# Kernel tuning notes

Measured on AMD Instinct MI355X. Metric: run time of the kernel, lower is better.

## Reference

```python
import jax, jax.numpy as jnp
import numpy as np

NUM_HEADS = 16
HEAD_DIM = 64  # hidden 1024 / 16 heads


def setup_inputs() -> dict:
    key = jax.random.key(0)
    ks = jax.random.split(key, 4)
    B, S, D = 2, 2048, 1024
    scale = 1.0 / np.sqrt(D)
    return {
        "hidden_states": jax.random.normal(ks[0], (B, S, D), jnp.float32),
        "Wq": jax.random.normal(ks[1], (D, D), jnp.float32) * scale,
        "bq": jnp.zeros((D,), jnp.float32),
        "Wk": jax.random.normal(ks[2], (D, D), jnp.float32) * scale,
        "bk": jnp.zeros((D,), jnp.float32),
        "Wv": jax.random.normal(ks[3], (D, D), jnp.float32) * scale,
        "bv": jnp.zeros((D,), jnp.float32),
    }


def _split_heads(x):
    B, S, D = x.shape
    return x.reshape(B, S, NUM_HEADS, HEAD_DIM).transpose(0, 2, 1, 3)  # [B,H,S,dh]


def reference(hidden_states, Wq, bq, Wk, bk, Wv, bv):
    q = _split_heads(hidden_states @ Wq + bq)
    k = _split_heads(hidden_states @ Wk + bk)
    v = _split_heads(hidden_states @ Wv + bv)
    scores = jnp.einsum("bhqd,bhkd->bhqk", q, k) / jnp.sqrt(
        jnp.asarray(HEAD_DIM, hidden_states.dtype))
    probs = jax.nn.softmax(scores, axis=-1)  # dropout is identity in eval mode
    ctx = jnp.einsum("bhqk,bhkd->bhqd", probs, v)
    B, H, S, dh = ctx.shape
    return ctx.transpose(0, 2, 1, 3).reshape(B, S, H * dh)
```

## Files before the change

### kernel.cpp

```cpp
#include <hip/hip_runtime.h>
#include <hip/hip_bf16.h>


typedef __attribute__((ext_vector_type(8))) short bf16x8;
typedef __attribute__((ext_vector_type(4))) float f32x4;
typedef __attribute__((ext_vector_type(4))) int int4v;

#define MFMA16(A, B, C) __builtin_amdgcn_mfma_f32_16x16x32_bf16((A), (B), (C), 0, 0, 0)

#if __has_builtin(__builtin_amdgcn_exp2f)
#define EXP2(x) __builtin_amdgcn_exp2f(x)
#else
#define EXP2(x) exp2f(x)
#endif

static __device__ __forceinline__ unsigned short f2bf(float f) {
    union { float f; unsigned int u; } v;
    v.f = f;
    unsigned int u = v.u;
    u += ((u >> 16) & 1u) + 0x7FFFu;
    return (unsigned short)(u >> 16);
}

static __device__ __forceinline__ void gload_lds16(const void* g, void* l) {
    __builtin_amdgcn_global_load_lds(
        (const __attribute__((address_space(1))) void*)g,
        (__attribute__((address_space(3))) void*)l, 16, 0, 0);
}

__global__ __launch_bounds__(256) void cast_hs(const float* __restrict__ in,
                                               unsigned short* __restrict__ out) {
    const size_t i = ((size_t)blockIdx.x * 256 + threadIdx.x) * 8;
    float4 a0 = *reinterpret_cast<const float4*>(in + i);
    float4 a1 = *reinterpret_cast<const float4*>(in + i + 4);
    unsigned short t[8];
    t[0] = f2bf(a0.x); t[1] = f2bf(a0.y); t[2] = f2bf(a0.z); t[3] = f2bf(a0.w);
    t[4] = f2bf(a1.x); t[5] = f2bf(a1.y); t[6] = f2bf(a1.z); t[7] = f2bf(a1.w);
    *reinterpret_cast<int4v*>(out + i) = *reinterpret_cast<int4v*>(t);
}

__global__ __launch_bounds__(256) void transpose_cast_w(
    const float* __restrict__ W0, const float* __restrict__ W1,
    const float* __restrict__ W2, unsigned short* __restrict__ Wt) {
    __shared__ float Ts[64][65];
    const float* W = (blockIdx.z == 0) ? W0 : (blockIdx.z == 1) ? W1 : W2;
    unsigned short* O = Wt + (size_t)blockIdx.z * 1048576;

    const int t  = threadIdx.x;
    const int k0 = blockIdx.y * 64;
    const int n0 = blockIdx.x * 64;

    {
        const int kr = t >> 2, nc = (t & 3) * 16;
        const float* p = W + (size_t)(k0 + kr) * 1024 + n0 + nc;
        float4 r0 = *reinterpret_cast<const float4*>(p);
        float4 r1 = *reinterpret_cast<const float4*>(p + 4);
        float4 r2 = *reinterpret_cast<const float4*>(p + 8);
        float4 r3 = *reinterpret_cast<const float4*>(p + 12);
        float* d = &Ts[kr][nc];
        d[0]=r0.x; d[1]=r0.y; d[2]=r0.z; d[3]=r0.w;
        d[4]=r1.x; d[5]=r1.y; d[6]=r1.z; d[7]=r1.w;
        d[8]=r2.x; d[9]=r2.y; d[10]=r2.z; d[11]=r2.w;
        d[12]=r3.x; d[13]=r3.y; d[14]=r3.z; d[15]=r3.w;
    }
    __syncthreads();
    {
        const int nr = t >> 2, kc = (t & 3) * 16;
        unsigned short tmp[16];
#pragma unroll
        for (int i = 0; i < 16; i++) tmp[i] = f2bf(Ts[kc + i][nr]);
        unsigned short* d = O + (size_t)(n0 + nr) * 1024 + k0 + kc;
        *reinterpret_cast<int4v*>(d)     = *reinterpret_cast<int4v*>(&tmp[0]);
        *reinterpret_cast<int4v*>(d + 8) = *reinterpret_cast<int4v*>(&tmp[8]);
    }
}

__global__ __launch_bounds__(256) void qkv_gemm_dma(
    const unsigned short* __restrict__ hsb,
    const unsigned short* __restrict__ Wt,
    const float* __restrict__ b0, const float* __restrict__ b1,
    const float* __restrict__ b2,
    unsigned short* __restrict__ Qo,
    unsigned short* __restrict__ Ko,
    unsigned short* __restrict__ Vto)
{
    __shared__ unsigned short As[128][32];
    __shared__ unsigned short Bs[128][32];

    const int z = blockIdx.z;
    const unsigned short* W = Wt + (size_t)z * 1048576;
    const float* bias = (z == 0) ? b0 : (z == 1) ? b1 : b2;

    const int tid  = threadIdx.x;
    const int lane = tid & 63;
    const int w    = tid >> 6;
    const int l15  = lane & 15;
    const int quad = lane >> 4;
    const int m0   = blockIdx.y * 128;
    const int n0   = blockIdx.x * 128;
    const int wm   = (w >> 1) * 64;
    const int wn   = (w & 1) * 64;

    const int drow = lane >> 2;
    const int dcol = (lane & 3) * 8;

    f32x4 acc[4][4];
#pragma unroll
    for (int i = 0; i < 4; i++)
#pragma unroll
        for (int j = 0; j < 4; j++)
            acc[i][j] = (f32x4){0.f, 0.f, 0.f, 0.f};

    for (int k0 = 0; k0 < 1024; k0 += 32) {
        __syncthreads();
#pragma unroll
        for (int p = 0; p < 2; p++) {
            const int s = w * 2 + p;
            gload_lds16(hsb + (size_t)(m0 + s * 16 + drow) * 1024 + k0 + dcol,
                        &As[s * 16][0]);
            gload_lds16(W   + (size_t)(n0 + s * 16 + drow) * 1024 + k0 + dcol,
                        &Bs[s * 16][0]);
        }
        __syncthreads();

        bf16x8 af[4], bfr[4];
#pragma unroll
        for (int i = 0; i < 4; i++)
            af[i] = *reinterpret_cast<const bf16x8*>(&As[wm + i * 16 + l15][quad * 8]);
#pragma unroll
        for (int j = 0; j < 4; j++)
            bfr[j] = *reinterpret_cast<const bf16x8*>(&Bs[wn + j * 16 + l15][quad * 8]);
#pragma unroll
        for (int i = 0; i < 4; i++)
#pragma unroll
            for (int j = 0; j < 4; j++)
                acc[i][j] = MFMA16(af[i], bfr[j], acc[i][j]);
    }

    if (z == 0) {
        const float qs = 0.18033688f;
#pragma unroll
        for (int i = 0; i < 4; i++) {
            const int mbase = m0 + wm + i * 16 + quad * 4;
#pragma unroll
            for (int j = 0; j < 4; j++) {
                const int n = n0 + wn + j * 16 + l15;
                const int h = n >> 6, d = n & 63;
                const float bn = bias[n];
#pragma unroll
                for (int r = 0; r < 4; r++) {
                    const int mm = mbase + r;
                    const int b = mm >> 11, s = mm & 2047;
                    Qo[(((size_t)(b * 16 + h) * 2048 + s) * 64) + d] =
                        f2bf((acc[i][j][r] + bn) * qs);
                }
            }
        }
    } else if (z == 1) {
#pragma unroll
        for (int i = 0; i < 4; i++) {
            const int mbase = m0 + wm + i * 16 + quad * 4;
#pragma unroll
            for (int j = 0; j < 4; j++) {
                const int n = n0 + wn + j * 16 + l15;
                const int h = n >> 6, d = n & 63;
                const float bn = bias[n];
#pragma unroll
                for (int r = 0; r < 4; r++) {
                    const int mm = mbase + r;
                    const int b = mm >> 11, s = mm & 2047;
                    const int dsw = ((((d >> 3) ^ (s & 7)) & 7) << 3) | (d & 7);
                    Ko[(((size_t)(b * 16 + h) * 2048 + s) * 64) + dsw] =
                        f2bf(acc[i][j][r] + bn);
                }
            }
        }
    } else {
#pragma unroll
        for (int i = 0; i < 4; i++) {
            const int mbase = m0 + wm + i * 16 + quad * 4;
            const int b = mbase >> 11, s0 = mbase & 2047;
#pragma unroll
            for (int j = 0; j < 4; j++) {
                const int n = n0 + wn + j * 16 + l15;
                const int h = n >> 6, d = n & 63;
                const float bn = bias[n];
                ushort4 v4;
                v4.x = f2bf(acc[i][j][0] + bn);
                v4.y = f2bf(acc[i][j][1] + bn);
                v4.z = f2bf(acc[i][j][2] + bn);
                v4.w = f2bf(acc[i][j][3] + bn);
                const int cs  = (s0 & 63) >> 3;
                const int ssw = (s0 & ~63) | (((cs ^ (d & 7)) & 7) << 3) | (s0 & 7);
                *reinterpret_cast<ushort4*>(
                    Vto + ((size_t)(b * 16 + h) * 64 + d) * 2048 + ssw) = v4;
            }
        }
    }
}

__global__ __launch_bounds__(256) void attn3(
    const unsigned short* __restrict__ Qg,
    const unsigned short* __restrict__ Kg,
    const unsigned short* __restrict__ Vtg,
    float* __restrict__ out)
{
    __shared__ unsigned short Ks[64][64];
    __shared__ unsigned short Vs[64][64];
    __shared__ unsigned short Ps[4][16][66];

    const int tid  = threadIdx.x;
    const int lane = tid & 63;
    const int w    = tid >> 6;
    const int l15  = lane & 15;
    const int quad = lane >> 4;

    const int q0 = blockIdx.x * 64;
    const int h  = blockIdx.y;
    const int b  = blockIdx.z;
    const size_t base = (size_t)(b * 16 + h) * 2048 * 64;
    const unsigned short* Qh  = Qg  + base;
    const unsigned short* Kh  = Kg  + base;
    const unsigned short* Vth = Vtg + base;

    const int drow = lane >> 3;
    const int dcol = (lane & 7) * 8;

    bf16x8 qf[2];
#pragma unroll
    for (int ks = 0; ks < 2; ks++)
        qf[ks] = *reinterpret_cast<const bf16x8*>(
            Qh + (size_t)(q0 + w * 16 + l15) * 64 + ks * 32 + quad * 8);

    f32x4 o[4];
#pragma unroll
    for (int t = 0; t < 4; t++) o[t] = (f32x4){0.f, 0.f, 0.f, 0.f};
    float rsum[4] = {0.f, 0.f, 0.f, 0.f};

    const int c0 = (((quad + 0) ^ (l15 & 7)) & 7) * 8;
    const int c1 = (((quad + 4) ^ (l15 & 7)) & 7) * 8;

    for (int kt = 0; kt < 32; kt++) {
        __syncthreads();
#pragma unroll
        for (int p = 0; p < 2; p++) {
            const int s = w * 2 + p;
            gload_lds16(Kh  + (size_t)kt * 4096 + (size_t)(s * 8 + drow) * 64 + dcol,
                        &Ks[s * 8][0]);
            gload_lds16(Vth + (size_t)(s * 8 + drow) * 2048 + kt * 64 + dcol,
                        &Vs[s * 8][0]);
        }
        __syncthreads();

#pragma unroll
        for (int t = 0; t < 4; t++) {
            f32x4 sc = (f32x4){0.f, 0.f, 0.f, 0.f};
            {
                bf16x8 kf = *reinterpret_cast<const bf16x8*>(&Ks[t * 16 + l15][c0]);
                sc = MFMA16(qf[0], kf, sc);
            }
            {
                bf16x8 kf = *reinterpret_cast<const bf16x8*>(&Ks[t * 16 + l15][c1]);
                sc = MFMA16(qf[1], kf, sc);
            }
#pragma unroll
            for (int r = 0; r < 4; r++) {
                const float p = EXP2(sc[r]);
                rsum[r] += p;
                Ps[w][quad * 4 + r][t * 16 + l15] = f2bf(p);
            }
        }

        __builtin_amdgcn_wave_barrier();

        bf16x8 pf[2];
#pragma unroll
        for (int ks = 0; ks < 2; ks++)
            pf[ks] = *reinterpret_cast<const bf16x8*>(&Ps[w][l15][ks * 32 + quad * 8]);
#pragma unroll
        for (int t = 0; t < 4; t++) {
            {
                bf16x8 vf = *reinterpret_cast<const bf16x8*>(&Vs[t * 16 + l15][c0]);
                o[t] = MFMA16(pf[0], vf, o[t]);
            }
            {
                bf16x8 vf = *reinterpret_cast<const bf16x8*>(&Vs[t * 16 + l15][c1]);
                o[t] = MFMA16(pf[1], vf, o[t]);
            }
        }
    }

#pragma unroll
    for (int off = 1; off < 16; off <<= 1)
#pragma unroll
        for (int r = 0; r < 4; r++)
            rsum[r] += __shfl_xor(rsum[r], off, 64);

#pragma unroll
    for (int t = 0; t < 4; t++) {
#pragma unroll
        for (int r = 0; r < 4; r++) {
            const int q = q0 + w * 16 + quad * 4 + r;
            const size_t oidx = (((size_t)b * 2048 + q) * 16 + h) * 64 + t * 16 + l15;
            out[oidx] = o[t][r] / rsum[r];
        }
    }
}

__global__ void fill_sentinel(float* out, int n, float pat) {
    int i = blockIdx.x * blockDim.x + threadIdx.x;
    if (i < n) out[i] = pat;
}

extern "C" void kernel_launch(void* const* d_in, const int* in_sizes, int n_in,
                              void* d_out, int out_size, void* d_ws, size_t ws_size,
                              hipStream_t stream) {
    const size_t n_hs  = (size_t)4096 * 1024;
    const size_t n_w   = (size_t)1024 * 1024;
    const size_t n_qkv = n_hs;
    const size_t need = (n_hs + 3 * n_w + 3 * n_qkv) * sizeof(unsigned short);

    bool order_ok = (n_in == 7) &&
        in_sizes[0] == 4194304 &&
        in_sizes[1] == 1048576 && in_sizes[2] == 1024 &&
        in_sizes[3] == 1048576 && in_sizes[4] == 1024 &&
        in_sizes[5] == 1048576 && in_sizes[6] == 1024;
    if (!order_ok || out_size != 4194304) {
        fill_sentinel<<<(out_size + 255) / 256, 256, 0, stream>>>(
            (float*)d_out, out_size, 4.0f);
        return;
    }
    if (ws_size < need) {
        fill_sentinel<<<(out_size + 255) / 256, 256, 0, stream>>>(
            (float*)d_out, out_size, 2.0f);
        return;
    }

    const float* hs = (const float*)d_in[0];
    const float* Wq = (const float*)d_in[1];
    const float* bq = (const float*)d_in[2];
    const float* Wk = (const float*)d_in[3];
    const float* bk = (const float*)d_in[4];
    const float* Wv = (const float*)d_in[5];
    const float* bv = (const float*)d_in[6];

    unsigned short* hsb = (unsigned short*)d_ws;
    unsigned short* Wt  = hsb + n_hs;
    unsigned short* Q   = Wt + 3 * n_w;
    unsigned short* K   = Q + n_qkv;
    unsigned short* Vt  = K + n_qkv;

    cast_hs<<<2048, 256, 0, stream>>>(hs, hsb);
    transpose_cast_w<<<dim3(16, 16, 3), 256, 0, stream>>>(Wq, Wk, Wv, Wt);

    dim3 g1(8, 32, 3);
    qkv_gemm_dma<<<g1, dim3(256), 0, stream>>>(hsb, Wt, bq, bk, bv, Q, K, Vt);

    dim3 g2(32, 16, 2);
    attn3<<<g2, dim3(256), 0, stream>>>(Q, K, Vt, (float*)d_out);
}
```

Baseline: 202.2 us.

## Widen GEMM and attention K tiles, pre-swizzle operands to avoid LDS conflicts

The QKV GEMM K-step grows from 32 to 64. The bf16 hidden states and transposed weights are now written with an XOR column swizzle, so the GEMM's LDS fragment reads avoid bank conflicts. The attention kernel loads 128 keys per tile instead of 64, which halves the number of block barriers. The bf16 rounding also drops round-to-nearest-even for a simpler round-half-up, which slightly changes numerics. Larger LDS tiles may lower occupancy.

Measured after the change: 204.8 us. No clear change (+1.3%).

```diff
diff --git a/kernel.cpp b/kernel.cpp
--- a/kernel.cpp
+++ b/kernel.cpp
@@ -17,9 +17,7 @@
 static __device__ __forceinline__ unsigned short f2bf(float f) {
     union { float f; unsigned int u; } v;
     v.f = f;
-    unsigned int u = v.u;
-    u += ((u >> 16) & 1u) + 0x7FFFu;
-    return (unsigned short)(u >> 16);
+    return (unsigned short)((v.u + 0x8000u) >> 16);
 }
 
 static __device__ __forceinline__ void gload_lds16(const void* g, void* l) {
@@ -30,13 +28,17 @@
 
 __global__ __launch_bounds__(256) void cast_hs(const float* __restrict__ in,
                                                unsigned short* __restrict__ out) {
-    const size_t i = ((size_t)blockIdx.x * 256 + threadIdx.x) * 8;
-    float4 a0 = *reinterpret_cast<const float4*>(in + i);
-    float4 a1 = *reinterpret_cast<const float4*>(in + i + 4);
+    const size_t flat = ((size_t)blockIdx.x * 256 + threadIdx.x) * 8;
+    const int m = (int)(flat >> 10);
+    const int k = (int)(flat & 1023);
+    float4 a0 = *reinterpret_cast<const float4*>(in + flat);
+    float4 a1 = *reinterpret_cast<const float4*>(in + flat + 4);
     unsigned short t[8];
     t[0] = f2bf(a0.x); t[1] = f2bf(a0.y); t[2] = f2bf(a0.z); t[3] = f2bf(a0.w);
     t[4] = f2bf(a1.x); t[5] = f2bf(a1.y); t[6] = f2bf(a1.z); t[7] = f2bf(a1.w);
-    *reinterpret_cast<int4v*>(out + i) = *reinterpret_cast<int4v*>(t);
+    const int csw = (((k >> 3) & 7) ^ (m & 7)) << 3;
+    *reinterpret_cast<int4v*>(out + (size_t)m * 1024 + (k & ~63) + csw) =
+        *reinterpret_cast<int4v*>(t);
 }
 
 __global__ __launch_bounds__(256) void transpose_cast_w(
@@ -69,9 +71,11 @@
         unsigned short tmp[16];
 #pragma unroll
         for (int i = 0; i < 16; i++) tmp[i] = f2bf(Ts[kc + i][nr]);
-        unsigned short* d = O + (size_t)(n0 + nr) * 1024 + k0 + kc;
-        *reinterpret_cast<int4v*>(d)     = *reinterpret_cast<int4v*>(&tmp[0]);
-        *reinterpret_cast<int4v*>(d + 8) = *reinterpret_cast<int4v*>(&tmp[8]);
+        unsigned short* base = O + (size_t)(n0 + nr) * 1024 + k0;
+        const int c0 = ((kc >> 3) ^ (nr & 7)) & 7;
+        const int c1 = (((kc >> 3) + 1) ^ (nr & 7)) & 7;
+        *reinterpret_cast<int4v*>(base + c0 * 8) = *reinterpret_cast<int4v*>(&tmp[0]);
+        *reinterpret_cast<int4v*>(base + c1 * 8) = *reinterpret_cast<int4v*>(&tmp[8]);
     }
 }
 
@@ -84,8 +88,8 @@
     unsigned short* __restrict__ Ko,
     unsigned short* __restrict__ Vto)
 {
-    __shared__ unsigned short As[128][32];
-    __shared__ unsigned short Bs[128][32];
+    __shared__ unsigned short As[128][64];
+    __shared__ unsigned short Bs[128][64];
 
     const int z = blockIdx.z;
     const unsigned short* W = Wt + (size_t)z * 1048576;
@@ -101,8 +105,8 @@
     const int wm   = (w >> 1) * 64;
     const int wn   = (w & 1) * 64;
 
-    const int drow = lane >> 2;
-    const int dcol = (lane & 3) * 8;
+    const int drow = lane >> 3;
+    const int dcol = (lane & 7) * 8;
 
     f32x4 acc[4][4];
 #pragma unroll
@@ -111,30 +115,36 @@
         for (int j = 0; j < 4; j++)
             acc[i][j] = (f32x4){0.f, 0.f, 0.f, 0.f};
 
-    for (int k0 = 0; k0 < 1024; k0 += 32) {
+    const int l7 = l15 & 7;
+
+    for (int k0 = 0; k0 < 1024; k0 += 64) {
         __syncthreads();
 #pragma unroll
-        for (int p = 0; p < 2; p++) {
-            const int s = w * 2 + p;
-            gload_lds16(hsb + (size_t)(m0 + s * 16 + drow) * 1024 + k0 + dcol,
-                        &As[s * 16][0]);
-            gload_lds16(W   + (size_t)(n0 + s * 16 + drow) * 1024 + k0 + dcol,
-                        &Bs[s * 16][0]);
+        for (int p = 0; p < 4; p++) {
+            const int seg = w * 4 + p;
+            gload_lds16(hsb + (size_t)(m0 + seg * 8 + drow) * 1024 + k0 + dcol,
+                        &As[seg * 8][0]);
+            gload_lds16(W   + (size_t)(n0 + seg * 8 + drow) * 1024 + k0 + dcol,
+                        &Bs[seg * 8][0]);
         }
         __syncthreads();
 
-        bf16x8 af[4], bfr[4];
-#pragma unroll
-        for (int i = 0; i < 4; i++)
-            af[i] = *reinterpret_cast<const bf16x8*>(&As[wm + i * 16 + l15][quad * 8]);
-#pragma unroll
-        for (int j = 0; j < 4; j++)
-            bfr[j] = *reinterpret_cast<const bf16x8*>(&Bs[wn + j * 16 + l15][quad * 8]);
-#pragma unroll
-        for (int i = 0; i < 4; i++)
+#pragma unroll
+        for (int kk = 0; kk < 64; kk += 32) {
+            const int csw = ((((kk >> 3) + quad) ^ l7) & 7) * 8;
+            bf16x8 af[4], bfr[4];
+#pragma unroll
+            for (int i = 0; i < 4; i++)
+                af[i] = *reinterpret_cast<const bf16x8*>(&As[wm + i * 16 + l15][csw]);
 #pragma unroll
             for (int j = 0; j < 4; j++)
-                acc[i][j] = MFMA16(af[i], bfr[j], acc[i][j]);
+                bfr[j] = *reinterpret_cast<const bf16x8*>(&Bs[wn + j * 16 + l15][csw]);
+#pragma unroll
+            for (int i = 0; i < 4; i++)
+#pragma unroll
+                for (int j = 0; j < 4; j++)
+                    acc[i][j] = MFMA16(af[i], bfr[j], acc[i][j]);
+        }
     }
 
     if (z == 0) {
@@ -199,14 +209,14 @@
     }
 }
 
-__global__ __launch_bounds__(256) void attn3(
+__global__ __launch_bounds__(256) void attn4(
     const unsigned short* __restrict__ Qg,
     const unsigned short* __restrict__ Kg,
     const unsigned short* __restrict__ Vtg,
     float* __restrict__ out)
 {
-    __shared__ unsigned short Ks[64][64];
-    __shared__ unsigned short Vs[64][64];
+    __shared__ unsigned short Ks[128][64];
+    __shared__ unsigned short Vs[64][128];
     __shared__ unsigned short Ps[4][16][66];
 
     const int tid  = threadIdx.x;
@@ -223,9 +233,6 @@
     const unsigned short* Kh  = Kg  + base;
     const unsigned short* Vth = Vtg + base;
 
-    const int drow = lane >> 3;
-    const int dcol = (lane & 7) * 8;
-
     bf16x8 qf[2];
 #pragma unroll
     for (int ks = 0; ks < 2; ks++)
@@ -240,53 +247,64 @@
     const int c0 = (((quad + 0) ^ (l15 & 7)) & 7) * 8;
     const int c1 = (((quad + 4) ^ (l15 & 7)) & 7) * 8;
 
-    for (int kt = 0; kt < 32; kt++) {
+    for (int kt = 0; kt < 16; kt++) {
         __syncthreads();
 #pragma unroll
-        for (int p = 0; p < 2; p++) {
-            const int s = w * 2 + p;
-            gload_lds16(Kh  + (size_t)kt * 4096 + (size_t)(s * 8 + drow) * 64 + dcol,
-                        &Ks[s * 8][0]);
-            gload_lds16(Vth + (size_t)(s * 8 + drow) * 2048 + kt * 64 + dcol,
-                        &Vs[s * 8][0]);
+        for (int p = 0; p < 4; p++) {
+            const int seg = w * 4 + p;
+            gload_lds16(Kh + (size_t)kt * 8192 +
+                            (size_t)(seg * 8 + (lane >> 3)) * 64 + (lane & 7) * 8,
+                        &Ks[seg * 8][0]);
+            gload_lds16(Vth + (size_t)(seg * 4 + (lane >> 4)) * 2048 +
+                            kt * 128 + (lane & 15) * 8,
+                        &Vs[seg * 4][0]);
         }
         __syncthreads();
 
 #pragma unroll
-        for (int t = 0; t < 4; t++) {
-            f32x4 sc = (f32x4){0.f, 0.f, 0.f, 0.f};
-            {
-                bf16x8 kf = *reinterpret_cast<const bf16x8*>(&Ks[t * 16 + l15][c0]);
-                sc = MFMA16(qf[0], kf, sc);
-            }
-            {
-                bf16x8 kf = *reinterpret_cast<const bf16x8*>(&Ks[t * 16 + l15][c1]);
-                sc = MFMA16(qf[1], kf, sc);
-            }
-#pragma unroll
-            for (int r = 0; r < 4; r++) {
-                const float p = EXP2(sc[r]);
-                rsum[r] += p;
-                Ps[w][quad * 4 + r][t * 16 + l15] = f2bf(p);
-            }
-        }
-
-        __builtin_amdgcn_wave_barrier();
-
-        bf16x8 pf[2];
-#pragma unroll
-        for (int ks = 0; ks < 2; ks++)
-            pf[ks] = *reinterpret_cast<const bf16x8*>(&Ps[w][l15][ks * 32 + quad * 8]);
-#pragma unroll
-        for (int t = 0; t < 4; t++) {
-            {
-                bf16x8 vf = *reinterpret_cast<const bf16x8*>(&Vs[t * 16 + l15][c0]);
-                o[t] = MFMA16(pf[0], vf, o[t]);
-            }
-            {
-                bf16x8 vf = *reinterpret_cast<const bf16x8*>(&Vs[t * 16 + l15][c1]);
-                o[t] = MFMA16(pf[1], vf, o[t]);
-            }
+        for (int u = 0; u < 2; u++) {
+#pragma unroll
+            for (int t = 0; t < 4; t++) {
+                f32x4 sc = (f32x4){0.f, 0.f, 0.f, 0.f};
+                {
+                    bf16x8 kf = *reinterpret_cast<const bf16x8*>(
+                        &Ks[u * 64 + t * 16 + l15][c0]);
+                    sc = MFMA16(qf[0], kf, sc);
+                }
+                {
+                    bf16x8 kf = *reinterpret_cast<const bf16x8*>(
+                        &Ks[u * 64 + t * 16 + l15][c1]);
+                    sc = MFMA16(qf[1], kf, sc);
+                }
+#pragma unroll
+                for (int r = 0; r < 4; r++) {
+                    const float p = EXP2(sc[r]);
+                    rsum[r] += p;
+                    Ps[w][quad * 4 + r][t * 16 + l15] = f2bf(p);
+                }
+            }
+
+            __builtin_amdgcn_wave_barrier();
+
+            bf16x8 pf[2];
+#pragma unroll
+            for (int ks = 0; ks < 2; ks++)
+                pf[ks] = *reinterpret_cast<const bf16x8*>(
+                    &Ps[w][l15][ks * 32 + quad * 8]);
+#pragma unroll
+            for (int t = 0; t < 4; t++) {
+                {
+                    bf16x8 vf = *reinterpret_cast<const bf16x8*>(
+                        &Vs[t * 16 + l15][u * 64 + c0]);
+                    o[t] = MFMA16(pf[0], vf, o[t]);
+                }
+                {
+                    bf16x8 vf = *reinterpret_cast<const bf16x8*>(
+                        &Vs[t * 16 + l15][u * 64 + c1]);
+                    o[t] = MFMA16(pf[1], vf, o[t]);
+                }
+            }
+            __builtin_amdgcn_wave_barrier();
         }
     }
 
@@ -357,5 +375,5 @@
     qkv_gemm_dma<<<g1, dim3(256), 0, stream>>>(hsb, Wt, bq, bk, bv, Q, K, Vt);
 
     dim3 g2(32, 16, 2);
-    attn3<<<g2, dim3(256), 0, stream>>>(Q, K, Vt, (float*)d_out);
-}
+    attn4<<<g2, dim3(256), 0, stream>>>(Q, K, Vt, (float*)d_out);
+}
```
